# Optimization experiments

Hardware: AMD Instinct MI355X
Metric: run time of the kernel (lower is better)

## Reference

```python
import jax, jax.numpy as jnp
import numpy as np

D = 1024  # output_dim
N_EXPERTS = 3


def setup_inputs() -> dict:
    key = jax.random.key(0)
    k1, k2, k3 = jax.random.split(key, 3)
    B = 65536
    x = jax.random.normal(k1, (B, 3 * D), dtype=jnp.float32)
    # nn.Linear default init scale ~ 1/sqrt(fan_in)
    w1 = jax.random.normal(k2, (3 * D, D), dtype=jnp.float32) / np.sqrt(3 * D)
    b1 = jnp.zeros((D,), dtype=jnp.float32)
    w2 = jax.random.normal(k3, (D, N_EXPERTS), dtype=jnp.float32) / np.sqrt(D)
    b2 = jnp.zeros((N_EXPERTS,), dtype=jnp.float32)
    return {"combined_pooled_feat": x, "w1": w1, "b1": b1, "w2": w2, "b2": b2, "k": 2}


def reference(combined_pooled_feat, w1, b1, w2, b2, k):
    # gate MLP: Linear -> GELU (exact, erf-based like torch default) -> Linear -> Softmax
    h = jax.nn.gelu(combined_pooled_feat @ w1 + b1, approximate=False)
    gates = jax.nn.softmax(h @ w2 + b2, axis=-1)  # [B, 3]
    kk = min(k, gates.shape[1])
    _, topk_idx = jax.lax.top_k(gates, kk)  # [B, kk]
    B = gates.shape[0]
    mask = jnp.zeros_like(gates).at[jnp.arange(B)[:, None], topk_idx].set(1.0)
    gated = gates * mask
    gated = gated / (gated.sum(axis=1, keepdims=True) + 1e-8)
    return (gated, mask)
```

## Files before the change

### kernel.cpp

```cpp
#include <hip/hip_runtime.h>
#include <hip/hip_fp16.h>
#include <stdint.h>

#define B_ROWS 65536
#define K_DIM 3072
#define N_DIM 1024

#define BM 128
#define BN 256
#define BK 64
#define NBLK 4
#define THREADS 512
#define KSTEPS (K_DIM / BK)
#define MARGIN 6.0e-3f
#define FB_CAP 8192

typedef _Float16 f16x8 __attribute__((ext_vector_type(8)));
typedef float f32x4 __attribute__((ext_vector_type(4)));

#define VMCNT0() asm volatile("s_waitcnt vmcnt(0)" ::: "memory")
#define LGKM0() asm volatile("s_waitcnt lgkmcnt(0)" ::: "memory")
#define SCHEDB() __builtin_amdgcn_sched_barrier(0)

__device__ __forceinline__ float gelu_exact(float v) {
  return 0.5f * v * (1.0f + erff(v * 0.7071067811865476f));
}

__device__ __forceinline__ void gld16(const void* g, void* l) {
  __builtin_amdgcn_global_load_lds(
      (const __attribute__((address_space(1))) void*)g,
      (__attribute__((address_space(3))) void*)l, 16, 0, 0);
}

__device__ __forceinline__ f16x8 cvt8(const float4 a, const float4 b) {
  f16x8 h;
  h[0] = (_Float16)a.x; h[1] = (_Float16)a.y; h[2] = (_Float16)a.z; h[3] = (_Float16)a.w;
  h[4] = (_Float16)b.x; h[5] = (_Float16)b.y; h[6] = (_Float16)b.z; h[7] = (_Float16)b.w;
  return h;
}

__global__ void k_w1t(const float* __restrict__ w1, _Float16* __restrict__ w1img,
                      int* __restrict__ fb_cnt) {
  if (blockIdx.x == 0 && blockIdx.y == 0 && threadIdx.x == 0) *fb_cnt = 0;
  __shared__ _Float16 lw[64][264];
  const int kt = blockIdx.x, nb = blockIdx.y;
  const int t = threadIdx.x;
  for (int r = 0; r < 64; ++r)
    lw[r][t] = (_Float16)w1[(size_t)(kt * 64 + r) * N_DIM + nb * 256 + t];
  __syncthreads();
  const size_t tbase = ((size_t)(nb * KSTEPS + kt)) << 14;
#pragma unroll
  for (int i = 0; i < 8; ++i) {
    const int U = i * 256 + t;
    const int row = U >> 3, su = U & 7;
    const int u = su ^ (row & 7);
    f16x8 v;
#pragma unroll
    for (int j = 0; j < 8; ++j) v[j] = lw[u * 8 + j][row];
    *(f16x8*)(w1img + tbase + (size_t)U * 8) = v;
  }
}

__global__ __launch_bounds__(THREADS, 4) void k_gemm(
    const float* __restrict__ x, const _Float16* __restrict__ w1img,
    const float* __restrict__ b1, const float* __restrict__ w2,
    float* __restrict__ partial) {
  __shared__ __align__(16) _Float16 As[BM * BK];
  __shared__ __align__(16) _Float16 Bds[2][BN * BK];

  const int t = threadIdx.x;
  const int lane = t & 63;
  const int wid = t >> 6;
  const int wr = wid >> 2, wc = wid & 3;
  const int l15 = lane & 15, lhi = lane >> 4;
  const int r7 = l15 & 7;

  const int bid = blockIdx.x;
  const int swz = (bid & 7) * ((B_ROWS / BM) * NBLK / 8) + (bid >> 3);
  const int nb = swz & (NBLK - 1);
  const int rb = swz >> 2;
  const int row0 = rb * BM;

  const int arow = t >> 2;
  const int aq = t & 3;
  const int as0 = ((2 * aq) ^ (arow & 7)) << 3;
  const int as1 = ((2 * aq + 1) ^ (arow & 7)) << 3;
  const float* xbase = x + (size_t)(row0 + arow) * K_DIM + aq * 16;

  const _Float16* bimg = w1img + ((size_t)(nb * KSTEPS) << 14);
  const int ldsb = wid << 11;

  const int aoff0 = (wr * 64 + l15) * 64;
  const int boff0 = (wc * 64 + l15) * 64;
  const int su0 = (lhi ^ r7) << 3;
  const int su1 = ((4 + lhi) ^ r7) << 3;

  f32x4 acc[4][4];
#pragma unroll
  for (int m = 0; m < 4; ++m)
#pragma unroll
    for (int n = 0; n < 4; ++n) acc[m][n] = (f32x4){0.f, 0.f, 0.f, 0.f};

  float4 av[4];

#define ISSUE_B(BNX, DST)                                                     \
  gld16((BNX) + ldsb + lane * 8, (DST) + ldsb);                               \
  gld16((BNX) + ldsb + 512 + lane * 8, (DST) + ldsb + 512);                   \
  gld16((BNX) + ldsb + 1024 + lane * 8, (DST) + ldsb + 1024);                 \
  gld16((BNX) + ldsb + 1536 + lane * 8, (DST) + ldsb + 1536);
#define ISSUE_A(K0)                                                           \
  {                                                                           \
    const float* xp = xbase + (K0);                                           \
    av[0] = *(const float4*)(xp);                                             \
    av[1] = *(const float4*)(xp + 4);                                         \
    av[2] = *(const float4*)(xp + 8);                                         \
    av[3] = *(const float4*)(xp + 12);                                        \
  }
#define WRITE_A()                                                             \
  *(f16x8*)(As + arow * 64 + as0) = cvt8(av[0], av[1]);                       \
  *(f16x8*)(As + arow * 64 + as1) = cvt8(av[2], av[3]);
#define COMPUTE(BCUR)                                                         \
  {                                                                           \
    f16x8 af[4], bf[4];                                                       \
    _Pragma("unroll") for (int m = 0; m < 4; ++m)                             \
        af[m] = *(const f16x8*)(As + aoff0 + m * 1024 + su0);                 \
    _Pragma("unroll") for (int n = 0; n < 4; ++n)                             \
        bf[n] = *(const f16x8*)((BCUR) + boff0 + n * 1024 + su0);             \
    __builtin_amdgcn_s_setprio(1);                                            \
    _Pragma("unroll") for (int m = 0; m < 4; ++m)                             \
        _Pragma("unroll") for (int n = 0; n < 4; ++n)                         \
            acc[m][n] = __builtin_amdgcn_mfma_f32_16x16x32_f16(               \
                af[m], bf[n], acc[m][n], 0, 0, 0);                            \
    __builtin_amdgcn_s_setprio(0);                                            \
    _Pragma("unroll") for (int m = 0; m < 4; ++m)                             \
        af[m] = *(const f16x8*)(As + aoff0 + m * 1024 + su1);                 \
    _Pragma("unroll") for (int n = 0; n < 4; ++n)                             \
        bf[n] = *(const f16x8*)((BCUR) + boff0 + n * 1024 + su1);             \
    __builtin_amdgcn_s_setprio(1);                                            \
    _Pragma("unroll") for (int m = 0; m < 4; ++m)                             \
        _Pragma("unroll") for (int n = 0; n < 4; ++n)                         \
            acc[m][n] = __builtin_amdgcn_mfma_f32_16x16x32_f16(               \
                af[m], bf[n], acc[m][n], 0, 0, 0);                            \
    __builtin_amdgcn_s_setprio(0);                                            \
  }

  ISSUE_A(0);
  SCHEDB();
  ISSUE_B(bimg, Bds[0]);
  SCHEDB();
  WRITE_A();
  VMCNT0();
  LGKM0();
  __syncthreads();

  int buf = 0;
  for (int kt = 0; kt < KSTEPS; ++kt) {
    if (kt < KSTEPS - 1) {
      ISSUE_A((kt + 1) * BK);
      SCHEDB();
      const _Float16* bnx = bimg + ((size_t)(kt + 1) << 14);
      ISSUE_B(bnx, Bds[buf ^ 1]);
      SCHEDB();
    }
    COMPUTE(Bds[buf]);
    __syncthreads();
    if (kt < KSTEPS - 1) {
      WRITE_A();
      VMCNT0();
      LGKM0();
    }
    __syncthreads();
    buf ^= 1;
  }

  float* pl = (float*)&As[0];
  float w2v[4][3], b1v[4];
  const int n0g = nb * BN;
#pragma unroll
  for (int n = 0; n < 4; ++n) {
    const int gc = n0g + wc * 64 + n * 16 + l15;
    b1v[n] = b1[gc];
    w2v[n][0] = w2[gc * 3 + 0];
    w2v[n][1] = w2[gc * 3 + 1];
    w2v[n][2] = w2[gc * 3 + 2];
  }
#pragma unroll
  for (int m = 0; m < 4; ++m) {
#pragma unroll
    for (int j = 0; j < 4; ++j) {
      float s0 = 0.f, s1 = 0.f, s2 = 0.f;
#pragma unroll
      for (int n = 0; n < 4; ++n) {
        const float g = gelu_exact(acc[m][n][j] + b1v[n]);
        s0 += g * w2v[n][0];
        s1 += g * w2v[n][1];
        s2 += g * w2v[n][2];
      }
#pragma unroll
      for (int off = 1; off < 16; off <<= 1) {
        s0 += __shfl_xor(s0, off, 64);
        s1 += __shfl_xor(s1, off, 64);
        s2 += __shfl_xor(s2, off, 64);
      }
      if (l15 == 0) {
        const int r = wr * 64 + m * 16 + lhi * 4 + j;
        pl[r * 12 + wc * 3 + 0] = s0;
        pl[r * 12 + wc * 3 + 1] = s1;
        pl[r * 12 + wc * 3 + 2] = s2;
      }
    }
  }
  __syncthreads();
  if (t < BM) {
#pragma unroll
    for (int e = 0; e < 3; ++e) {
      partial[(size_t)(row0 + t) * 12 + nb * 3 + e] =
          pl[t * 12 + e] + pl[t * 12 + 3 + e] + pl[t * 12 + 6 + e] + pl[t * 12 + 9 + e];
    }
  }
#undef ISSUE_B
#undef ISSUE_A
#undef WRITE_A
#undef COMPUTE
}

__device__ __forceinline__ void gate_store(float* __restrict__ out, int r,
                                           float l0, float l1, float l2, int kk) {
  const float mx = fmaxf(l0, fmaxf(l1, l2));
  const float e0 = expf(l0 - mx), e1 = expf(l1 - mx), e2 = expf(l2 - mx);
  const float s = e0 + e1 + e2;
  const float g0 = e0 / s, g1 = e1 / s, g2 = e2 / s;
  const int r0 = (g1 > g0) + (g2 > g0);
  const int r1 = (g0 >= g1) + (g2 > g1);
  const int r2 = (g0 >= g2) + (g1 >= g2);
  const float m0 = (r0 < kk) ? 1.f : 0.f;
  const float m1 = (r1 < kk) ? 1.f : 0.f;
  const float m2 = (r2 < kk) ? 1.f : 0.f;
  const float ks = g0 * m0 + g1 * m1 + g2 * m2;
  const float inv = 1.f / (ks + 1e-8f);
  float* go = out + (size_t)r * 3;
  go[0] = g0 * m0 * inv;
  go[1] = g1 * m1 * inv;
  go[2] = g2 * m2 * inv;
  float* mo = out + (size_t)B_ROWS * 3 + (size_t)r * 3;
  mo[0] = m0;
  mo[1] = m1;
  mo[2] = m2;
}

__global__ void k_gate(const float* __restrict__ partial, const float* __restrict__ b2,
                       const int* __restrict__ kp, float* __restrict__ out,
                       int* __restrict__ fb_cnt, int* __restrict__ fb_rows) {
  const int r = blockIdx.x * blockDim.x + threadIdx.x;
  if (r >= B_ROWS) return;
  const float* p = partial + (size_t)r * 12;
  float l0 = b2[0], l1 = b2[1], l2 = b2[2];
#pragma unroll
  for (int c = 0; c < 4; ++c) {
    l0 += p[c * 3 + 0];
    l1 += p[c * 3 + 1];
    l2 += p[c * 3 + 2];
  }
  int kk = *kp;
  kk = kk < 3 ? kk : 3;
  gate_store(out, r, l0, l1, l2, kk);
  const float mx = fmaxf(l0, fmaxf(l1, l2));
  const float mn = fminf(l0, fminf(l1, l2));
  const float mid = l0 + l1 + l2 - mx - mn;
  float gap = 1e30f;
  if (kk == 1) gap = mx - mid;
  else if (kk == 2) gap = mid - mn;
  if (gap < MARGIN) {
    const int i = atomicAdd(fb_cnt, 1);
    if (i < FB_CAP) fb_rows[i] = r;
  }
}

__global__ __launch_bounds__(256) void k_fb_gemm(
    const float* __restrict__ x, const float* __restrict__ w1,
    const float* __restrict__ b1, const float* __restrict__ w2,
    const int* __restrict__ fb_cnt, const int* __restrict__ fb_rows,
    float* __restrict__ fb_partial) {
  int count = *fb_cnt;
  count = count < FB_CAP ? count : FB_CAP;
  if (count == 0) return;
  const int nc = blockIdx.y, n0 = nc * 64;
  const int t = threadIdx.x, col = t & 63, wrow = t >> 6;
  __shared__ float Xs[32][64];
  __shared__ float Ws[64][64];
  for (int slot = blockIdx.x; slot * 32 < count; slot += gridDim.x) {
    float accr[8] = {0.f, 0.f, 0.f, 0.f, 0.f, 0.f, 0.f, 0.f};
    for (int kt = 0; kt < K_DIM / 64; ++kt) {
      const int k0 = kt * 64;
      __syncthreads();
#pragma unroll
      for (int i = 0; i < 2; ++i) {
        const int idx = i * 256 + t, rr = idx >> 4, c4 = (idx & 15) << 2;
        int gi = slot * 32 + rr;
        gi = gi < count ? gi : count - 1;
        *(float4*)&Xs[rr][c4] = *(const float4*)(x + (size_t)fb_rows[gi] * K_DIM + k0 + c4);
      }
#pragma unroll
      for (int i = 0; i < 4; ++i) {
        const int idx = i * 256 + t, rr = idx >> 4, c4 = (idx & 15) << 2;
        *(float4*)&Ws[rr][c4] = *(const float4*)(w1 + (size_t)(k0 + rr) * N_DIM + n0 + c4);
      }
      __syncthreads();
#pragma unroll 4
      for (int kk = 0; kk < 64; ++kk) {
        const float wv = Ws[kk][col];
#pragma unroll
        for (int rr = 0; rr < 8; ++rr) accr[rr] += Xs[wrow * 8 + rr][kk] * wv;
      }
    }
    const float bv = b1[n0 + col];
    const float w20 = w2[(n0 + col) * 3 + 0];
    const float w21 = w2[(n0 + col) * 3 + 1];
    const float w22 = w2[(n0 + col) * 3 + 2];
#pragma unroll
    for (int rr = 0; rr < 8; ++rr) {
      const float g = gelu_exact(accr[rr] + bv);
      float c0 = g * w20, c1 = g * w21, c2 = g * w22;
#pragma unroll
      for (int off = 1; off < 64; off <<= 1) {
        c0 += __shfl_xor(c0, off, 64);
        c1 += __shfl_xor(c1, off, 64);
        c2 += __shfl_xor(c2, off, 64);
      }
      const int gi = slot * 32 + wrow * 8 + rr;
      if (col == 0 && gi < count) {
        float* fp = fb_partial + ((size_t)gi * 16 + nc) * 3;
        fp[0] = c0;
        fp[1] = c1;
        fp[2] = c2;
      }
    }
  }
}

__global__ void k_fb_fin(const float* __restrict__ fb_partial, const float* __restrict__ b2,
                         const int* __restrict__ kp, const int* __restrict__ fb_cnt,
                         const int* __restrict__ fb_rows, float* __restrict__ out) {
  const int i = blockIdx.x * blockDim.x + threadIdx.x;
  int count = *fb_cnt;
  count = count < FB_CAP ? count : FB_CAP;
  if (i >= count) return;
  const int r = fb_rows[i];
  float l0 = b2[0], l1 = b2[1], l2 = b2[2];
  const float* fp = fb_partial + (size_t)i * 48;
#pragma unroll
  for (int c = 0; c < 16; ++c) {
    l0 += fp[c * 3 + 0];
    l1 += fp[c * 3 + 1];
    l2 += fp[c * 3 + 2];
  }
  int kk = *kp;
  kk = kk < 3 ? kk : 3;
  gate_store(out, r, l0, l1, l2, kk);
}

extern "C" void kernel_launch(void* const* d_in, const int* in_sizes, int n_in,
                              void* d_out, int out_size, void* d_ws, size_t ws_size,
                              hipStream_t stream) {
  (void)in_sizes; (void)n_in; (void)out_size; (void)ws_size;
  const float* x  = (const float*)d_in[0];
  const float* w1 = (const float*)d_in[1];
  const float* b1 = (const float*)d_in[2];
  const float* w2 = (const float*)d_in[3];
  const float* b2 = (const float*)d_in[4];
  const int*   kp = (const int*)d_in[5];
  float* out = (float*)d_out;

  uint8_t* ws = (uint8_t*)d_ws;
  _Float16* w1img   = (_Float16*)(ws);
  float* partial    = (float*)(ws + 6291456);
  int* fb_cnt       = (int*)(ws + 9437184);
  int* fb_rows      = (int*)(ws + 9437440);
  float* fb_partial = (float*)(ws + 9470208);

  k_w1t<<<dim3(KSTEPS, NBLK), 256, 0, stream>>>(w1, w1img, fb_cnt);
  k_gemm<<<dim3((B_ROWS / BM) * NBLK), THREADS, 0, stream>>>(x, w1img, b1, w2, partial);
  k_gate<<<dim3(B_ROWS / 256), 256, 0, stream>>>(partial, b2, kp, out, fb_cnt, fb_rows);
  k_fb_gemm<<<dim3(16, 16), 256, 0, stream>>>(x, w1, b1, w2, fb_cnt, fb_rows, fb_partial);
  k_fb_fin<<<dim3(FB_CAP / 256), 256, 0, stream>>>(fb_partial, b2, kp, fb_cnt, fb_rows, out);
}
```

Measured before the change: 744.5 us.

## Double GEMM row tile to 256 and peel last k-step from main loop

Raises the row tile of the main GEMM from 128 to 256, so each wave accumulates 8x4 MFMA tiles and each B tile in LDS is reused over twice as many rows. Each thread now loads 32 floats of x per step, and occupancy is lowered to 2 workgroups per CU. The last k-step is peeled out of the loop, which removes the per-iteration branches, and __syncthreads is swapped for raw s_barrier with explicit waits. The aim is less B-tile traffic per FLOP and fewer workgroups, at the cost of more registers, LDS and latency-hiding pressure.

```diff
diff --git a/kernel.cpp b/kernel.cpp
--- a/kernel.cpp
+++ b/kernel.cpp
@@ -6,7 +6,7 @@
 #define K_DIM 3072
 #define N_DIM 1024
 
-#define BM 128
+#define BM 256
 #define BN 256
 #define BK 64
 #define NBLK 4
@@ -14,10 +14,12 @@
 #define KSTEPS (K_DIM / BK)
 #define MARGIN 6.0e-3f
 #define FB_CAP 8192
+#define NWG ((B_ROWS / BM) * NBLK)
 
 typedef _Float16 f16x8 __attribute__((ext_vector_type(8)));
 typedef float f32x4 __attribute__((ext_vector_type(4)));
 
+#define BARR() __builtin_amdgcn_s_barrier()
 #define VMCNT0() asm volatile("s_waitcnt vmcnt(0)" ::: "memory")
 #define LGKM0() asm volatile("s_waitcnt lgkmcnt(0)" ::: "memory")
 #define SCHEDB() __builtin_amdgcn_sched_barrier(0)
@@ -61,7 +63,7 @@
   }
 }
 
-__global__ __launch_bounds__(THREADS, 4) void k_gemm(
+__global__ __launch_bounds__(THREADS, 2) void k_gemm(
     const float* __restrict__ x, const _Float16* __restrict__ w1img,
     const float* __restrict__ b1, const float* __restrict__ w2,
     float* __restrict__ partial) {
@@ -76,103 +78,94 @@
   const int r7 = l15 & 7;
 
   const int bid = blockIdx.x;
-  const int swz = (bid & 7) * ((B_ROWS / BM) * NBLK / 8) + (bid >> 3);
+  const int swz = (bid & 7) * (NWG / 8) + (bid >> 3);
   const int nb = swz & (NBLK - 1);
   const int rb = swz >> 2;
   const int row0 = rb * BM;
 
-  const int arow = t >> 2;
-  const int aq = t & 3;
-  const int as0 = ((2 * aq) ^ (arow & 7)) << 3;
-  const int as1 = ((2 * aq + 1) ^ (arow & 7)) << 3;
-  const float* xbase = x + (size_t)(row0 + arow) * K_DIM + aq * 16;
+  const int arow = t >> 1;
+  const int aq = t & 1;
+  const float* xbase = x + (size_t)(row0 + arow) * K_DIM + aq * 32;
+  int asl[4];
+#pragma unroll
+  for (int i = 0; i < 4; ++i) asl[i] = ((aq * 4 + i) ^ (arow & 7)) << 3;
 
   const _Float16* bimg = w1img + ((size_t)(nb * KSTEPS) << 14);
   const int ldsb = wid << 11;
 
-  const int aoff0 = (wr * 64 + l15) * 64;
+  const int aoff0 = (wr * 128 + l15) * 64;
   const int boff0 = (wc * 64 + l15) * 64;
   const int su0 = (lhi ^ r7) << 3;
   const int su1 = ((4 + lhi) ^ r7) << 3;
 
-  f32x4 acc[4][4];
-#pragma unroll
-  for (int m = 0; m < 4; ++m)
+  f32x4 acc[8][4];
+#pragma unroll
+  for (int m = 0; m < 8; ++m)
 #pragma unroll
     for (int n = 0; n < 4; ++n) acc[m][n] = (f32x4){0.f, 0.f, 0.f, 0.f};
 
-  float4 av[4];
-
-#define ISSUE_B(BNX, DST)                                                     \
-  gld16((BNX) + ldsb + lane * 8, (DST) + ldsb);                               \
-  gld16((BNX) + ldsb + 512 + lane * 8, (DST) + ldsb + 512);                   \
-  gld16((BNX) + ldsb + 1024 + lane * 8, (DST) + ldsb + 1024);                 \
-  gld16((BNX) + ldsb + 1536 + lane * 8, (DST) + ldsb + 1536);
+  float4 av[8];
+
+#define ISSUE_B(KT, DST)                                                      \
+  {                                                                           \
+    const _Float16* bnx = bimg + ((size_t)(KT) << 14);                        \
+    gld16(bnx + ldsb + lane * 8, (DST) + ldsb);                               \
+    gld16(bnx + ldsb + 512 + lane * 8, (DST) + ldsb + 512);                   \
+    gld16(bnx + ldsb + 1024 + lane * 8, (DST) + ldsb + 1024);                 \
+    gld16(bnx + ldsb + 1536 + lane * 8, (DST) + ldsb + 1536);                 \
+  }
 #define ISSUE_A(K0)                                                           \
   {                                                                           \
     const float* xp = xbase + (K0);                                           \
-    av[0] = *(const float4*)(xp);                                             \
-    av[1] = *(const float4*)(xp + 4);                                         \
-    av[2] = *(const float4*)(xp + 8);                                         \
-    av[3] = *(const float4*)(xp + 12);                                        \
+    _Pragma("unroll") for (int i = 0; i < 8; ++i)                             \
+        av[i] = *(const float4*)(xp + i * 4);                                 \
   }
 #define WRITE_A()                                                             \
-  *(f16x8*)(As + arow * 64 + as0) = cvt8(av[0], av[1]);                       \
-  *(f16x8*)(As + arow * 64 + as1) = cvt8(av[2], av[3]);
-#define COMPUTE(BCUR)                                                         \
+  _Pragma("unroll") for (int i = 0; i < 4; ++i)                               \
+      *(f16x8*)(As + arow * 64 + asl[i]) = cvt8(av[2 * i], av[2 * i + 1]);
+#define HALF(BCUR, SU)                                                        \
   {                                                                           \
-    f16x8 af[4], bf[4];                                                       \
-    _Pragma("unroll") for (int m = 0; m < 4; ++m)                             \
-        af[m] = *(const f16x8*)(As + aoff0 + m * 1024 + su0);                 \
+    f16x8 af[8], bf[4];                                                       \
+    _Pragma("unroll") for (int m = 0; m < 8; ++m)                             \
+        af[m] = *(const f16x8*)(As + aoff0 + m * 1024 + (SU));                \
     _Pragma("unroll") for (int n = 0; n < 4; ++n)                             \
-        bf[n] = *(const f16x8*)((BCUR) + boff0 + n * 1024 + su0);             \
+        bf[n] = *(const f16x8*)((BCUR) + boff0 + n * 1024 + (SU));            \
     __builtin_amdgcn_s_setprio(1);                                            \
-    _Pragma("unroll") for (int m = 0; m < 4; ++m)                             \
+    _Pragma("unroll") for (int m = 0; m < 8; ++m)                             \
         _Pragma("unroll") for (int n = 0; n < 4; ++n)                         \
             acc[m][n] = __builtin_amdgcn_mfma_f32_16x16x32_f16(               \
                 af[m], bf[n], acc[m][n], 0, 0, 0);                            \
     __builtin_amdgcn_s_setprio(0);                                            \
-    _Pragma("unroll") for (int m = 0; m < 4; ++m)                             \
-        af[m] = *(const f16x8*)(As + aoff0 + m * 1024 + su1);                 \
-    _Pragma("unroll") for (int n = 0; n < 4; ++n)                             \
-        bf[n] = *(const f16x8*)((BCUR) + boff0 + n * 1024 + su1);             \
-    __builtin_amdgcn_s_setprio(1);                                            \
-    _Pragma("unroll") for (int m = 0; m < 4; ++m)                             \
-        _Pragma("unroll") for (int n = 0; n < 4; ++n)                         \
-            acc[m][n] = __builtin_amdgcn_mfma_f32_16x16x32_f16(               \
-                af[m], bf[n], acc[m][n], 0, 0, 0);                            \
-    __builtin_amdgcn_s_setprio(0);                                            \
   }
 
   ISSUE_A(0);
   SCHEDB();
-  ISSUE_B(bimg, Bds[0]);
+  ISSUE_B(0, Bds[0]);
   SCHEDB();
   WRITE_A();
   VMCNT0();
   LGKM0();
-  __syncthreads();
+  BARR();
 
   int buf = 0;
-  for (int kt = 0; kt < KSTEPS; ++kt) {
-    if (kt < KSTEPS - 1) {
-      ISSUE_A((kt + 1) * BK);
-      SCHEDB();
-      const _Float16* bnx = bimg + ((size_t)(kt + 1) << 14);
-      ISSUE_B(bnx, Bds[buf ^ 1]);
-      SCHEDB();
-    }
-    COMPUTE(Bds[buf]);
-    __syncthreads();
-    if (kt < KSTEPS - 1) {
-      WRITE_A();
-      VMCNT0();
-      LGKM0();
-    }
-    __syncthreads();
+  for (int kt = 0; kt < KSTEPS - 1; ++kt) {
+    ISSUE_A((kt + 1) * BK);
+    SCHEDB();
+    ISSUE_B(kt + 1, Bds[buf ^ 1]);
+    SCHEDB();
+    HALF(Bds[buf], su0);
+    HALF(Bds[buf], su1);
+    BARR();
+    WRITE_A();
+    VMCNT0();
+    LGKM0();
+    BARR();
     buf ^= 1;
   }
-
+  HALF(Bds[buf], su0);
+  HALF(Bds[buf], su1);
+
+  BARR();
   float* pl = (float*)&As[0];
   float w2v[4][3], b1v[4];
   const int n0g = nb * BN;
@@ -185,7 +178,7 @@
     w2v[n][2] = w2[gc * 3 + 2];
   }
 #pragma unroll
-  for (int m = 0; m < 4; ++m) {
+  for (int m = 0; m < 8; ++m) {
 #pragma unroll
     for (int j = 0; j < 4; ++j) {
       float s0 = 0.f, s1 = 0.f, s2 = 0.f;
@@ -203,14 +196,15 @@
         s2 += __shfl_xor(s2, off, 64);
       }
       if (l15 == 0) {
-        const int r = wr * 64 + m * 16 + lhi * 4 + j;
+        const int r = wr * 128 + m * 16 + lhi * 4 + j;
         pl[r * 12 + wc * 3 + 0] = s0;
         pl[r * 12 + wc * 3 + 1] = s1;
         pl[r * 12 + wc * 3 + 2] = s2;
       }
     }
   }
-  __syncthreads();
+  LGKM0();
+  BARR();
   if (t < BM) {
 #pragma unroll
     for (int e = 0; e < 3; ++e) {
@@ -221,7 +215,7 @@
 #undef ISSUE_B
 #undef ISSUE_A
 #undef WRITE_A
-#undef COMPUTE
+#undef HALF
 }
 
 __device__ __forceinline__ void gate_store(float* __restrict__ out, int r,
@@ -379,7 +373,7 @@
   float* fb_partial = (float*)(ws + 9470208);
 
   k_w1t<<<dim3(KSTEPS, NBLK), 256, 0, stream>>>(w1, w1img, fb_cnt);
-  k_gemm<<<dim3((B_ROWS / BM) * NBLK), THREADS, 0, stream>>>(x, w1img, b1, w2, partial);
+  k_gemm<<<dim3(NWG), THREADS, 0, stream>>>(x, w1img, b1, w2, partial);
   k_gate<<<dim3(B_ROWS / 256), 256, 0, stream>>>(partial, b2, kp, out, fb_cnt, fb_rows);
   k_fb_gemm<<<dim3(16, 16), 256, 0, stream>>>(x, w1, b1, w2, fb_cnt, fb_rows, fb_partial);
   k_fb_fin<<<dim3(FB_CAP / 256), 256, 0, stream>>>(fb_partial, b2, kp, fb_cnt, fb_rows, out);
```

Measured after the change: 1.062 ms. 1.43x slower.
